# Performance work log

Hardware: AMD Instinct MI355X
Metric: run time of the kernel (lower is better)

Reference implementation:

```python
import jax, jax.numpy as jnp
import numpy as np

N, C_IN, H, W = 32, 256, 56, 56
C_OUT, KH, KW = 256, 3, 3
ACT_BITS = 8


def setup_inputs() -> dict:
    key = jax.random.key(0)
    k_x, k_w, k_s, k_b = jax.random.split(key, 4)
    x = jax.random.normal(k_x, (N, C_IN, H, W), dtype=jnp.float32)
    # ternary weights in {-1, 0, +1}, stored as int8
    w_q = jax.random.randint(k_w, (C_OUT, C_IN, KH, KW), -1, 2).astype(jnp.int8)
    # per-output-channel scale, broadcastable over NCHW as [C,1,1]
    s = (jax.random.uniform(k_s, (C_OUT, 1, 1), dtype=jnp.float32) * 0.02 + 0.005)
    bias = jax.random.normal(k_b, (C_OUT,), dtype=jnp.float32) * 0.1
    act_s = jnp.float32(1.0 / 127.0)  # per-tensor activation quant scale
    return {"x": x, "w_q": w_q, "s": s, "bias": bias, "act_s": act_s}


def reference(x, w_q, s, bias, act_s):
    # activation fake-quant: clamp to [-1,1], round to act_bits symmetric grid
    qmax = (1 << (ACT_BITS - 1)) - 1  # 127
    x = jnp.clip(x, -1.0, 1.0)
    x_int = jnp.clip(jnp.round(x / act_s), -qmax, qmax)
    xq = x_int * act_s
    # ternary conv (weights upcast to float), stride 1, pad 1, dilation 1
    y = jax.lax.conv_general_dilated(
        xq, w_q.astype(jnp.float32),
        window_strides=(1, 1), padding=((1, 1), (1, 1)),
        lhs_dilation=(1, 1), rhs_dilation=(1, 1),
        dimension_numbers=("NCHW", "OIHW", "NCHW"), feature_group_count=1)
    # per-output-channel scale + bias
    y = y * s + bias.reshape(1, -1, 1, 1)
    return y
```

## Files before the change

### kernel.cpp

```cpp
#include <hip/hip_runtime.h>

typedef int v4i __attribute__((ext_vector_type(4)));

#define NIMG 32
#define CIN  256
#define COUT 256
#define HW   3136
#define W56  56
#define HP   58
#define PIMG (HP * HP)
#define XQP_BYTES (NIMG * PIMG * CIN)
#define WP_BYTES  (9 * COUT * CIN)

#define BARRIER() asm volatile("s_barrier" ::: "memory")
#define VMCNT0()  asm volatile("s_waitcnt vmcnt(0)" ::: "memory")

__global__ __launch_bounds__(256) void zero_border(v4i* __restrict__ p)
{
    int i = blockIdx.x * 256 + threadIdx.x;
    if (i >= NIMG * 228 * 16) return;
    int n = i / 3648, r = i % 3648, pix = r >> 4, c = r & 15;
    int h, w;
    if (pix < 58)       { h = 0;         w = pix;       }
    else if (pix < 116) { h = 57;        w = pix - 58;  }
    else if (pix < 172) { h = pix - 115; w = 0;         }
    else                { h = pix - 171; w = 57;        }
    v4i z = {0, 0, 0, 0};
    p[(size_t)(n * PIMG + h * HP + w) * 16 + c] = z;
}

__global__ __launch_bounds__(256) void quantize_pad(
    const float* __restrict__ x, signed char* __restrict__ xqp)
{
    __shared__ int tile[64][65];
    const int n  = blockIdx.z;
    const int c0 = blockIdx.y * 64;
    const int p0 = blockIdx.x * 64;
    const int tid = threadIdx.x;

    const int px   = tid & 63;
    const int crow = tid >> 6;
    const float* xb = x + ((size_t)(n * CIN + c0)) * HW + p0;
#pragma unroll
    for (int i = 0; i < 16; ++i) {
        int c = crow + i * 4;
        float v = xb[(size_t)c * HW + px];
        v = fminf(fmaxf(v, -1.f), 1.f);
        tile[c][px] = (int)rintf(v * 127.f);
    }
    __syncthreads();

    const int c4   = tid & 15;
    const int prow = tid >> 4;
#pragma unroll
    for (int i = 0; i < 4; ++i) {
        int p  = prow + i * 16;
        int hw = p0 + p;
        int oh = hw / W56, ow = hw % W56;
        int b0 = tile[c4 * 4 + 0][p] & 255;
        int b1 = tile[c4 * 4 + 1][p] & 255;
        int b2 = tile[c4 * 4 + 2][p] & 255;
        int b3 = tile[c4 * 4 + 3][p] & 255;
        int packed = b0 | (b1 << 8) | (b2 << 16) | (b3 << 24);
        *(int*)(xqp + ((size_t)(n * PIMG + (oh + 1) * HP + (ow + 1))) * CIN
                    + c0 + c4 * 4) = packed;
    }
}

__global__ __launch_bounds__(256) void repack_w(
    const int* __restrict__ wq, signed char* __restrict__ wp2)
{
    int idx  = blockIdx.x * 256 + threadIdx.x;
    int t    = idx >> 16;
    int rem  = idx & 65535;
    int kc   = rem >> 14;
    int rem2 = rem & 16383;
    int co   = rem2 >> 6;
    int c6   = rem2 & 63;
    int ci   = kc * 64 + c6;
    wp2[idx] = (signed char)wq[(co * CIN + ci) * 9 + t];
}

__device__ __forceinline__ void gll16(const void* g, void* l)
{
    __builtin_amdgcn_global_load_lds(
        (const __attribute__((address_space(1))) int*)g,
        (__attribute__((address_space(3))) int*)l, 16, 0, 0);
}

__device__ __forceinline__ int boffset(int ss)
{
    int t9 = ss >> 2, kc = ss & 3;
    return ((t9 / 3 - 1) * HP + (t9 % 3 - 1)) * CIN + kc * 64;
}

__global__ __launch_bounds__(256) void bitconv_mfma(
    const signed char* __restrict__ xqp, const signed char* __restrict__ wp2,
    const float* __restrict__ s_, const float* __restrict__ bias,
    const float* __restrict__ act_s_p, float* __restrict__ out)
{
    __shared__ signed char lds[2][32768];

    const int tid  = threadIdx.x;
    const int lane = tid & 63;
    const int wid  = tid >> 6;
    const int wr   = wid >> 1;
    const int wc   = wid & 1;
    const int l15  = lane & 15;
    const int kg   = lane >> 4;
    const int kgs  = ((kg ^ ((l15 >> 1) & 3)) << 4);

    const int b  = blockIdx.x;
    const int w  = (b & 7) * 196 + (b >> 3);
    const int px0   = (w >> 1) * 128;
    const int cout0 = (w & 1) * 128;

    const int srow   = tid >> 2;
    const int schunk = (((tid & 3) ^ ((tid >> 3) & 3)) << 4);
    const signed char* asrc = wp2 + cout0 * 64 + srow * 64 + schunk;

    const signed char* bsrc[2];
#pragma unroll
    for (int r = 0; r < 2; ++r) {
        int p = px0 + srow + r * 64;
        int n = p / HW, q = p % HW;
        bsrc[r] = xqp
            + ((size_t)(n * PIMG + (q / W56 + 1) * HP + (q % W56 + 1))) * CIN
            + schunk;
    }

    int aoff[4], boff[4];
#pragma unroll
    for (int i = 0; i < 4; ++i)
        aoff[i] = (wr * 64 + i * 16 + l15) * 64 + kgs;
#pragma unroll
    for (int j = 0; j < 4; ++j)
        boff[j] = 8192 + (wc * 64 + j * 16 + l15) * 64 + kgs;

    v4i acc[4][4] = {};

    const int wb = wid * 1024;

    auto stage = [&](int buf, int t) {
        signed char* L = &lds[buf][0];
#pragma unroll
        for (int h = 0; h < 2; ++h) {
            const int ss = 2 * t + h;
            const signed char* a = asrc + ss * 16384;
            const int R = h * 16384;
            gll16(a,        L + R + wb);
            gll16(a + 4096, L + R + 4096 + wb);
            int bo = boffset(ss);
            gll16(bsrc[0] + bo, L + R + 8192  + wb);
            gll16(bsrc[1] + bo, L + R + 12288 + wb);
        }
    };

    stage(0, 0);
    VMCNT0();
    BARRIER();

    for (int it = 0; it < 9; ++it) {
#pragma unroll
        for (int u = 0; u < 2; ++u) {
            const int t = it * 2 + u;
            const signed char* L = &lds[u][0];

            if (t < 17) stage(u ^ 1, t + 1);

            v4i a[4], bb[4];
#pragma unroll
            for (int i = 0; i < 4; ++i) a[i]  = *(const v4i*)(L + aoff[i]);
#pragma unroll
            for (int j = 0; j < 4; ++j) bb[j] = *(const v4i*)(L + boff[j]);

            __builtin_amdgcn_s_setprio(1);
#pragma unroll
            for (int i = 0; i < 4; ++i)
#pragma unroll
                for (int j = 0; j < 4; ++j)
                    acc[i][j] = __builtin_amdgcn_mfma_i32_16x16x64_i8(
                        a[i], bb[j], acc[i][j], 0, 0, 0);
            __builtin_amdgcn_s_setprio(0);

            v4i a2[4], bb2[4];
#pragma unroll
            for (int i = 0; i < 4; ++i) a2[i]  = *(const v4i*)(L + 16384 + aoff[i]);
#pragma unroll
            for (int j = 0; j < 4; ++j) bb2[j] = *(const v4i*)(L + 16384 + boff[j]);

            __builtin_amdgcn_s_setprio(1);
#pragma unroll
            for (int i = 0; i < 4; ++i)
#pragma unroll
                for (int j = 0; j < 4; ++j)
                    acc[i][j] = __builtin_amdgcn_mfma_i32_16x16x64_i8(
                        a2[i], bb2[j], acc[i][j], 0, 0, 0);
            __builtin_amdgcn_s_setprio(0);

            if (t < 17) {
                VMCNT0();
                BARRIER();
            }
        }
    }

    const float a_s = act_s_p[0];
    int nn[4], hh[4];
#pragma unroll
    for (int j = 0; j < 4; ++j) {
        int op = px0 + wc * 64 + j * 16 + l15;
        nn[j] = op / HW;
        hh[j] = op % HW;
    }
#pragma unroll
    for (int i = 0; i < 4; ++i) {
        int cb = cout0 + wr * 64 + i * 16 + kg * 4;
        float sc[4], bi[4];
#pragma unroll
        for (int r = 0; r < 4; ++r) {
            sc[r] = a_s * s_[cb + r];
            bi[r] = bias[cb + r];
        }
#pragma unroll
        for (int j = 0; j < 4; ++j)
#pragma unroll
            for (int r = 0; r < 4; ++r)
                out[((size_t)(nn[j] * COUT + cb + r)) * HW + hh[j]] =
                    (float)acc[i][j][r] * sc[r] + bi[r];
    }
}

extern "C" void kernel_launch(void* const* d_in, const int* in_sizes, int n_in,
                              void* d_out, int out_size, void* d_ws, size_t ws_size,
                              hipStream_t stream)
{
    const float* x     = (const float*)d_in[0];
    const int*   w_q   = (const int*)d_in[1];
    const float* s     = (const float*)d_in[2];
    const float* bias  = (const float*)d_in[3];
    const float* act_s = (const float*)d_in[4];

    signed char* xqp = (signed char*)d_ws;
    signed char* wp2 = (signed char*)d_ws + XQP_BYTES;

    zero_border<<<(NIMG * 228 * 16 + 255) / 256, 256, 0, stream>>>((v4i*)xqp);
    quantize_pad<<<dim3(49, 4, NIMG), 256, 0, stream>>>(x, xqp);
    repack_w<<<dim3(WP_BYTES / 256), 256, 0, stream>>>(w_q, wp2);
    bitconv_mfma<<<dim3(1568), 256, 0, stream>>>(
        xqp, wp2, s, bias, act_s, (float*)d_out);
}
```

Before: 99.29 us.

## Triple-buffer LDS per K-step and prefetch MFMA fragments into registers

The main loop moves from double-buffered LDS stages of two K-slices to a three-buffer ring of single K-slices, with global-to-LDS loads issued two steps ahead. Fragments for the next step are read from LDS into a second register set before the current MFMAs run, so LDS read latency overlaps with matrix math. LDS use drops from 64KB to 48KB, which may allow more resident blocks. The cost is twice as many wait-plus-barrier points per tile and more live registers for the duplicated fragments.

Result: slower. 112.8 us (+13.6%).

```diff
diff --git a/kernel.cpp b/kernel.cpp
--- a/kernel.cpp
+++ b/kernel.cpp
@@ -99,7 +99,7 @@
     const float* __restrict__ s_, const float* __restrict__ bias,
     const float* __restrict__ act_s_p, float* __restrict__ out)
 {
-    __shared__ signed char lds[2][32768];
+    __shared__ signed char lds[3][16384];
 
     const int tid  = threadIdx.x;
     const int lane = tid & 63;
@@ -138,41 +138,46 @@
         boff[j] = 8192 + (wc * 64 + j * 16 + l15) * 64 + kgs;
 
     v4i acc[4][4] = {};
+    v4i fa[2][4], fb[2][4];
 
     const int wb = wid * 1024;
 
-    auto stage = [&](int buf, int t) {
+    auto stage = [&](int buf, int ss) {
         signed char* L = &lds[buf][0];
-#pragma unroll
-        for (int h = 0; h < 2; ++h) {
-            const int ss = 2 * t + h;
-            const signed char* a = asrc + ss * 16384;
-            const int R = h * 16384;
-            gll16(a,        L + R + wb);
-            gll16(a + 4096, L + R + 4096 + wb);
-            int bo = boffset(ss);
-            gll16(bsrc[0] + bo, L + R + 8192  + wb);
-            gll16(bsrc[1] + bo, L + R + 12288 + wb);
-        }
+        const signed char* a = asrc + ss * 16384;
+        gll16(a,        L + wb);
+        gll16(a + 4096, L + 4096 + wb);
+        int bo = boffset(ss);
+        gll16(bsrc[0] + bo, L + 8192  + wb);
+        gll16(bsrc[1] + bo, L + 12288 + wb);
     };
 
     stage(0, 0);
+    stage(1, 1);
     VMCNT0();
     BARRIER();
-
-    for (int it = 0; it < 9; ++it) {
-#pragma unroll
-        for (int u = 0; u < 2; ++u) {
-            const int t = it * 2 + u;
-            const signed char* L = &lds[u][0];
-
-            if (t < 17) stage(u ^ 1, t + 1);
-
-            v4i a[4], bb[4];
-#pragma unroll
-            for (int i = 0; i < 4; ++i) a[i]  = *(const v4i*)(L + aoff[i]);
-#pragma unroll
-            for (int j = 0; j < 4; ++j) bb[j] = *(const v4i*)(L + boff[j]);
+#pragma unroll
+    for (int i = 0; i < 4; ++i) fa[0][i] = *(const v4i*)(&lds[0][0] + aoff[i]);
+#pragma unroll
+    for (int j = 0; j < 4; ++j) fb[0][j] = *(const v4i*)(&lds[0][0] + boff[j]);
+
+    for (int it = 0; it < 6; ++it) {
+#pragma unroll
+        for (int u = 0; u < 6; ++u) {
+            const int s  = it * 6 + u;
+            const int cu = u & 1;
+            const int nx = cu ^ 1;
+            const int nbf = (u + 1) % 3;
+
+            if (s < 34) stage((u + 2) % 3, s + 2);
+
+            if (s < 35) {
+                const signed char* L = &lds[nbf][0];
+#pragma unroll
+                for (int i = 0; i < 4; ++i) fa[nx][i] = *(const v4i*)(L + aoff[i]);
+#pragma unroll
+                for (int j = 0; j < 4; ++j) fb[nx][j] = *(const v4i*)(L + boff[j]);
+            }
 
             __builtin_amdgcn_s_setprio(1);
 #pragma unroll
@@ -180,25 +185,10 @@
 #pragma unroll
                 for (int j = 0; j < 4; ++j)
                     acc[i][j] = __builtin_amdgcn_mfma_i32_16x16x64_i8(
-                        a[i], bb[j], acc[i][j], 0, 0, 0);
+                        fa[cu][i], fb[cu][j], acc[i][j], 0, 0, 0);
             __builtin_amdgcn_s_setprio(0);
 
-            v4i a2[4], bb2[4];
-#pragma unroll
-            for (int i = 0; i < 4; ++i) a2[i]  = *(const v4i*)(L + 16384 + aoff[i]);
-#pragma unroll
-            for (int j = 0; j < 4; ++j) bb2[j] = *(const v4i*)(L + 16384 + boff[j]);
-
-            __builtin_amdgcn_s_setprio(1);
-#pragma unroll
-            for (int i = 0; i < 4; ++i)
-#pragma unroll
-                for (int j = 0; j < 4; ++j)
-                    acc[i][j] = __builtin_amdgcn_mfma_i32_16x16x64_i8(
-                        a2[i], bb2[j], acc[i][j], 0, 0, 0);
-            __builtin_amdgcn_s_setprio(0);
-
-            if (t < 17) {
+            if (s < 35) {
                 VMCNT0();
                 BARRIER();
             }
```
